# Optimization experiments

Hardware: AMD Instinct MI355X
Metric: run time of the kernel (lower is better)

## Reference

```python
import jax, jax.numpy as jnp
import numpy as np

B, N, C = 16, 2048, 128
NCLS = 40


def setup_inputs() -> dict:
    key = jax.random.key(0)
    ks = iter(jax.random.split(key, 40))

    def nrm(shape, s=0.05):
        return jax.random.normal(next(ks), shape, dtype=jnp.float32) * s

    return {
        "x": jax.random.normal(next(ks), (B, 3, N), dtype=jnp.float32),
        "conv1_w": nrm((128, 3), 0.5),
        "bn1_g": jnp.ones((128,), jnp.float32), "bn1_b": jnp.zeros((128,), jnp.float32),
        "conv2_w": nrm((128, 128)),
        "bn2_g": jnp.ones((128,), jnp.float32), "bn2_b": jnp.zeros((128,), jnp.float32),
        "sa_wqk": nrm((4, 32, 128)),
        "sa_wv": nrm((4, 128, 128)), "sa_bv": nrm((4, 128)),
        "sa_wt": nrm((4, 128, 128)), "sa_bt": nrm((4, 128)),
        "sa_g": jnp.ones((4, 128), jnp.float32), "sa_b": jnp.zeros((4, 128), jnp.float32),
        "fuse_w": nrm((1024, 512)),
        "fuse_g": jnp.ones((1024,), jnp.float32), "fuse_b": jnp.zeros((1024,), jnp.float32),
        "lin1_w": nrm((512, 1024)),
        "bn6_g": jnp.ones((512,), jnp.float32), "bn6_b": jnp.zeros((512,), jnp.float32),
        "lin2_w": nrm((256, 512)), "lin2_b": jnp.zeros((256,), jnp.float32),
        "bn7_g": jnp.ones((256,), jnp.float32), "bn7_b": jnp.zeros((256,), jnp.float32),
        "lin3_w": nrm((NCLS, 256)), "lin3_b": jnp.zeros((NCLS,), jnp.float32),
    }


def _pconv(w, x):
    # 1x1 Conv1d == channel matmul: [O,C] x [B,C,N] -> [B,O,N]
    return jnp.einsum('oc,bcn->bon', w, x)


def _fwd(x, conv1_w, bn1_g, bn1_b, conv2_w, bn2_g, bn2_b,
         sa_wqk, sa_wv, sa_bv, sa_wt, sa_bt, sa_g, sa_b,
         fuse_w, fuse_g, fuse_b, lin1_w, bn6_g, bn6_b,
         lin2_w, lin2_b, bn7_g, bn7_b, lin3_w, lin3_b):
    # conv stem (BN in eval mode: running mean=0, var=1 -> affine)
    h = jax.nn.relu(bn1_g[:, None] * _pconv(conv1_w, x) + bn1_b[:, None])
    h = jax.nn.relu(bn2_g[:, None] * _pconv(conv2_w, h) + bn2_b[:, None])

    outs = []
    for i in range(4):  # fixed number of structurally identical SA blocks
        # q_conv and k_conv share the same weight (aliased in the torch code)
        q = jnp.einsum('dc,bcn->bdn', sa_wqk[i], h)           # [B,32,N]
        energy = jnp.einsum('bdi,bdj->bij', q, q)             # [B,N,N]
        att = jax.nn.softmax(energy, axis=-1)
        att = att / (1e-9 + att.sum(axis=1, keepdims=True))   # extra L1 renorm over dim=1
        v = _pconv(sa_wv[i], h) + sa_bv[i][:, None]           # [B,C,N]
        x_r = jnp.einsum('bcn,bnm->bcm', v, att)              # [B,C,N]
        t = _pconv(sa_wt[i], h - x_r) + sa_bt[i][:, None]
        h = h + jax.nn.relu(sa_g[i][:, None] * t + sa_b[i][:, None])
        outs.append(h)

    cat = jnp.concatenate(outs, axis=1)                        # [B,512,N]
    f = fuse_g[:, None] * _pconv(fuse_w, cat) + fuse_b[:, None]
    f = jnp.where(f > 0, f, 0.2 * f)                           # LeakyReLU(0.2)
    g = f.max(axis=-1)                                         # adaptive max pool -> [B,1024]

    h1 = jax.nn.relu(bn6_g * (g @ lin1_w.T) + bn6_b)           # dropout = identity (eval)
    h2 = jax.nn.relu(bn7_g * (h1 @ lin2_w.T + lin2_b) + bn7_b)
    return h2 @ lin3_w.T + lin3_b                              # [B,40]


def reference(x, conv1_w, bn1_g, bn1_b, conv2_w, bn2_g, bn2_b,
              sa_wqk, sa_wv, sa_bv, sa_wt, sa_bt, sa_g, sa_b,
              fuse_w, fuse_g, fuse_b, lin1_w, bn6_g, bn6_b,
              lin2_w, lin2_b, bn7_g, bn7_b, lin3_w, lin3_b):
    return _fwd(x, conv1_w, bn1_g, bn1_b, conv2_w, bn2_g, bn2_b,
                sa_wqk, sa_wv, sa_bv, sa_wt, sa_bt, sa_g, sa_b,
                fuse_w, fuse_g, fuse_b, lin1_w, bn6_g, bn6_b,
                lin2_w, lin2_b, bn7_g, bn7_b, lin3_w, lin3_b)
```

## Files before the change

kernel.cpp:

```cpp
#include <hip/hip_runtime.h>

typedef __attribute__((ext_vector_type(4))) float f4;
typedef __attribute__((ext_vector_type(8))) short s16x8;
typedef __attribute__((ext_vector_type(4))) unsigned short us4;
typedef __attribute__((ext_vector_type(2))) unsigned int u32x2;
typedef unsigned short u16;
typedef unsigned int u32;

#define DEVI __device__ __forceinline__

DEVI u16 f2bf(float f){
    u32 u = __builtin_bit_cast(u32, f);
    u32 r = (u + 0x7fffu + ((u >> 16) & 1u)) >> 16;
    return (u16)r;
}
DEVI f4 mfma16(s16x8 a, s16x8 b, f4 c){
    return __builtin_amdgcn_mfma_f32_16x16x32_bf16(a, b, c, 0, 0, 0);
}
DEVI u32 cvtpk(float lo, float hi){
    u32 r;
    asm("v_cvt_pk_bf16_f32 %0, %1, %2" : "=v"(r) : "v"(lo), "v"(hi));
    return r;
}
DEVI void gload(const u16* g, u16* l){
    __builtin_amdgcn_global_load_lds((const __attribute__((address_space(1))) void*)g,
                                     (__attribute__((address_space(3))) void*)l, 16, 0, 0);
}

#define L2E 1.44269504088896340736f

__global__ __launch_bounds__(256) void k_cast(const float* w2, const float* wqk,
                                              const float* wv, const float* wt,
                                              const float* wf, u16* out){
    int i = blockIdx.x * 256 + threadIdx.x;
    if(i < 16384)       out[i] = f2bf(w2[i]);
    else if(i < 32768)  out[i] = f2bf(wqk[i - 16384]);
    else if(i < 98304)  out[i] = f2bf(wv[i - 32768]);
    else if(i < 163840) out[i] = f2bf(wt[i - 98304]);
    else if(i < 688128){
        int t = i - 163840;
        int o = t >> 9, c = t & 511;
        int jg = o >> 4, l15 = o & 15, ks = c >> 5, kr = c & 31;
        out[163840 + (size_t)(jg*16 + ks)*512 + l15*32 + kr] = f2bf(wf[t]);
    }
}

__global__ __launch_bounds__(256) void k_stem1(const float* x, const float* w1,
                                               const float* g1, const float* b1, u16* h1tb){
    int t = blockIdx.x * 256 + threadIdx.x;
    int b = t >> 11, n = t & 2047;
    const float* xb = x + (size_t)b * 3 * 2048 + n;
    float x0 = xb[0], x1 = xb[2048], x2 = xb[4096];
    u32* o = (u32*)(h1tb + (size_t)t * 128);
    #pragma unroll 8
    for(int c = 0; c < 128; c += 2){
        float a0 = fmaxf(g1[c]   * (w1[c*3+0]*x0 + w1[c*3+1]*x1 + w1[c*3+2]*x2) + b1[c],   0.f);
        float a1 = fmaxf(g1[c+1] * (w1[c*3+3]*x0 + w1[c*3+4]*x1 + w1[c*3+5]*x2) + b1[c+1], 0.f);
        o[c >> 1] = (u32)f2bf(a0) | ((u32)f2bf(a1) << 16);
    }
}

DEVI int swz512(int bid){ return ((bid & 7) << 6) | (bid >> 3); }
DEVI int swz1024(int bid){ return ((bid & 7) << 7) | (bid >> 3); }

DEVI void qv_phase(const u16* T, const u16* wqkb, const u16* wvb, const float* bv,
                   u16* qb, u16* vt, int b, int n0, int wv_, int l15, int kg){
    f4 accv[8], accq[2];
    #pragma unroll
    for(int j=0;j<8;j++) accv[j] = (f4){0.f,0.f,0.f,0.f};
    accq[0] = (f4){0.f,0.f,0.f,0.f}; accq[1] = accq[0];
    int row = wv_*16 + l15;
    #pragma unroll
    for(int ks=0; ks<4; ks++){
        s16x8 a = *(const s16x8*)&T[row*128 + ((ks*32 + kg*8) ^ ((row&7)<<3))];
        #pragma unroll
        for(int j=0;j<8;j++){
            s16x8 bb = *(const s16x8*)(wvb + (size_t)(j*16 + l15)*128 + ks*32 + kg*8);
            accv[j] = mfma16(a, bb, accv[j]);
        }
        #pragma unroll
        for(int f=0; f<2; f++){
            s16x8 wf_ = *(const s16x8*)(wqkb + (size_t)(f*16 + l15)*128 + ks*32 + kg*8);
            accq[f] = mfma16(wf_, a, accq[f]);
        }
    }
    int nb = n0 + wv_*16;
    int it = nb >> 5;
    int k0 = (nb & 31) + kg*4;
    int vbase = ((k0 >> 3)*16)*8 + (k0 & 7);
    #pragma unroll
    for(int j=0;j<8;j++){
        float bvo = bv[j*16 + l15];
        us4 pk;
        #pragma unroll
        for(int r=0;r<4;r++) pk[r] = f2bf(accv[j][r] + bvo);
        *(us4*)(vt + (size_t)((b*64 + it)*8 + j)*512 + vbase + l15*8) = pk;
    }
    int n = n0 + wv_*16 + l15;
    #pragma unroll
    for(int f=0; f<2; f++){
        us4 pk;
        #pragma unroll
        for(int r=0;r<4;r++) pk[r] = f2bf(accq[f][r]);
        *(us4*)(qb + (size_t)(b*2048 + n)*32 + f*16 + kg*4) = pk;
    }
}

__global__ __launch_bounds__(256) void k_conv2qv(const u16* h1tb, const u16* w2b,
                                                 const float* g2, const float* b2,
                                                 float* ht0,
                                                 const u16* wqkb, const u16* wvb,
                                                 const float* bv, u16* qb, u16* vt){
    __shared__ u16 T[8192];
    int bid2 = swz512(blockIdx.x);
    int b = bid2 >> 5;
    int n0 = (bid2 & 31) << 6;
    int lane = threadIdx.x & 63, wv_ = threadIdx.x >> 6;
    int l15 = lane & 15, kg = lane >> 4;
    const u16* arow = h1tb + (size_t)(b*2048 + n0 + wv_*16 + l15) * 128 + kg*8;
    f4 acc[8];
    #pragma unroll
    for(int j=0;j<8;j++) acc[j] = (f4){0.f,0.f,0.f,0.f};
    #pragma unroll
    for(int ks=0; ks<4; ks++){
        s16x8 a = *(const s16x8*)(arow + ks*32);
        #pragma unroll
        for(int j=0;j<8;j++){
            s16x8 bb = *(const s16x8*)(w2b + (size_t)(j*16 + l15)*128 + ks*32 + kg*8);
            acc[j] = mfma16(a, bb, acc[j]);
        }
    }
    int nn0 = n0 + wv_*16 + kg*4;
    #pragma unroll
    for(int j=0;j<8;j++){
        int o = j*16 + l15;
        float gg = g2[o], be = b2[o];
        #pragma unroll
        for(int r=0;r<4;r++){
            float h = fmaxf(gg * acc[j][r] + be, 0.f);
            int nl = wv_*16 + kg*4 + r;
            ht0[(size_t)(b*2048 + nn0 + r) * 128 + o] = h;
            T[nl*128 + (o ^ ((nl&7)<<3))] = f2bf(h);
        }
    }
    __syncthreads();
    qv_phase(T, wqkb, wvb, bv, qb, vt, b, n0, wv_, l15, kg);
}

__global__ __launch_bounds__(256) void k_passA(const u16* qb, float* crowp){
    int bid2 = swz1024(blockIdx.x);
    int b = bid2 >> 6;
    int rest = bid2 & 63;
    int i0 = (rest >> 1) << 6;
    int jh = rest & 1;
    int jbeg = jh << 10;
    int lane = threadIdx.x & 63, wv_ = threadIdx.x >> 6;
    int l15 = lane & 15, kg = lane >> 4;
    const u16* qbase = qb + (size_t)b * 2048 * 32;
    s16x8 af = *(const s16x8*)(qbase + (size_t)(i0 + wv_*16 + l15)*32 + kg*8);
    float m[4], s[4], mml[4];
    const f4 z = {0.f,0.f,0.f,0.f};
    {
        s16x8 b0 = *(const s16x8*)(qbase + (size_t)(jbeg + l15)*32 + kg*8);
        s16x8 b1 = *(const s16x8*)(qbase + (size_t)(jbeg + 16 + l15)*32 + kg*8);
        f4 e0 = mfma16(af, b0, z);
        f4 e1 = mfma16(af, b1, z);
        #pragma unroll
        for(int r=0;r<4;r++){
            m[r] = fmaxf(e0[r], e1[r]);
            mml[r] = -m[r]*L2E;
            s[r] = exp2f(fmaf(e0[r], L2E, mml[r])) + exp2f(fmaf(e1[r], L2E, mml[r]));
        }
    }
    for(int j0=jbeg+32; j0<jbeg+1024; j0+=32){
        s16x8 b0 = *(const s16x8*)(qbase + (size_t)(j0 + l15)*32 + kg*8);
        s16x8 b1 = *(const s16x8*)(qbase + (size_t)(j0 + 16 + l15)*32 + kg*8);
        f4 e0 = mfma16(af, b0, z);
        f4 e1 = mfma16(af, b1, z);
        #pragma unroll
        for(int r=0;r<4;r++){
            float mx = fmaxf(e0[r], e1[r]);
            if(mx > m[r] + 8.f){
                s[r] *= exp2f((m[r]-mx)*L2E);
                m[r] = mx; mml[r] = -mx*L2E;
            }
            s[r] += exp2f(fmaf(e0[r], L2E, mml[r])) + exp2f(fmaf(e1[r], L2E, mml[r]));
        }
    }
    #pragma unroll
    for(int d=1; d<16; d<<=1){
        #pragma unroll
        for(int r=0;r<4;r++){
            float mo = __shfl_xor(m[r], d);
            float so = __shfl_xor(s[r], d);
            float mn = fmaxf(m[r], mo);
            s[r] = s[r]*exp2f((m[r]-mn)*L2E) + so*exp2f((mo-mn)*L2E);
            m[r] = mn;
        }
    }
    if(l15 == 0){
        #pragma unroll
        for(int r=0;r<4;r++){
            int i = i0 + wv_*16 + kg*4 + r;
            crowp[jh*32768 + b*2048 + i] = m[r]*L2E + log2f(s[r]);
        }
    }
}

__global__ __launch_bounds__(512) void k_passB(const u16* qb, const u16* vt,
                                               const float* crowp,
                                               const float* hprev, int ldh,
                                               u16* dtb){
    __shared__ u16 V[2][8192];
    __shared__ u16 P[2][4096];
    __shared__ float CR[2048];
    __shared__ float csl[2][64];
    int bid2 = swz512(blockIdx.x);
    int b = bid2 >> 5;
    int j0 = (bid2 & 31) << 6;
    int tid = threadIdx.x;
    int lane = tid & 63, wv_ = tid >> 6;
    int jw = wv_ >> 1, ih = wv_ & 1;
    int l15 = lane & 15, kg = lane >> 4;
    int jh = jw * 16;
    const u16* qbase = qb + (size_t)b * 2048 * 32;
    const u16* vtb = vt + (size_t)b * 64*8*512;

    #pragma unroll
    for(int p=0;p<4;p++){
        int i = p*512 + tid;
        float c0 = crowp[b*2048 + i], c1 = crowp[32768 + b*2048 + i];
        float mx = fmaxf(c0, c1), mn = fminf(c0, c1);
        CR[i] = mx + log2f(1.f + exp2f(mn - mx));
    }

    s16x8 eb = *(const s16x8*)(qbase + (size_t)(j0 + jh + l15)*32 + kg*8);
    f4 acc[8];
    #pragma unroll
    for(int j=0;j<8;j++) acc[j] = (f4){0.f,0.f,0.f,0.f};
    float csp = 0.f;
    const f4 z = {0.f,0.f,0.f,0.f};

    auto stage = [&](int ic, int buf){
        const u16* src = vtb + (size_t)ic*8192 + wv_*1024 + lane*8;
        u16* dst = &V[buf][wv_*1024];
        gload(src, dst);
        gload(src + 512, dst + 512);
    };
    auto eph = [&](int ic, int buf){
        #pragma unroll
        for(int is=0; is<2; is++){
            int isub = ih*2 + is;
            s16x8 ea = *(const s16x8*)(qbase + (size_t)(ic*64 + isub*16 + l15)*32 + kg*8);
            f4 e = mfma16(ea, eb, z);
            f4 cc = *(const f4*)&CR[ic*64 + isub*16 + kg*4];
            float q0 = exp2f(fmaf(e[0], L2E, -cc[0]));
            float q1 = exp2f(fmaf(e[1], L2E, -cc[1]));
            float q2 = exp2f(fmaf(e[2], L2E, -cc[2]));
            float q3 = exp2f(fmaf(e[3], L2E, -cc[3]));
            csp += q0 + q1 + q2 + q3;
            u32x2 pk = { cvtpk(q0, q1), cvtpk(q2, q3) };
            int idx = wv_*512 + ((is*2 + (kg>>1))*16 + l15)*8 + (kg&1)*4;
            *(u32x2*)&P[buf][idx] = pk;
        }
    };

    __syncthreads();
    stage(0, 0);
    eph(0, 0);
    __syncthreads();
    for(int it=0; it<32; it++){
        int cur = it & 1;
        if(it < 31){ stage(it+1, cur^1); eph(it+1, cur^1); }
        s16x8 pa = *(const s16x8*)&P[cur][wv_*512 + lane*8];
        __builtin_amdgcn_s_setprio(1);
        #pragma unroll
        for(int jc=0;jc<8;jc++){
            s16x8 vf = *(const s16x8*)&V[cur][ih*4096 + jc*512 + lane*8];
            acc[jc] = mfma16(pa, vf, acc[jc]);
        }
        __builtin_amdgcn_s_setprio(0);
        __syncthreads();
    }
    csp += __shfl_xor(csp, 16);
    csp += __shfl_xor(csp, 32);
    if(lane < 16) csl[ih][jh + l15] = csp;
    __syncthreads();
    float* comb = (float*)V;
    if(ih == 1){
        #pragma unroll
        for(int jc=0;jc<8;jc++)
            *(f4*)&comb[jw*2048 + jc*256 + lane*4] = acc[jc];
    }
    __syncthreads();
    if(ih == 0){
        #pragma unroll
        for(int jc=0;jc<8;jc++){
            f4 o = *(const f4*)&comb[jw*2048 + jc*256 + lane*4];
            acc[jc][0] += o[0]; acc[jc][1] += o[1];
            acc[jc][2] += o[2]; acc[jc][3] += o[3];
        }
        #pragma unroll
        for(int r=0;r<4;r++){
            int jr = jh + kg*4 + r;
            float inv = 1.0f / (1e-9f + csl[0][jr] + csl[1][jr]);
            int n = j0 + jr;
            const float* hrow = hprev + (size_t)(b*2048 + n)*ldh;
            u16* drow = dtb + (size_t)(b*2048 + n)*128;
            #pragma unroll
            for(int jc=0;jc<8;jc++){
                int c = jc*16 + l15;
                drow[c] = f2bf(hrow[c] - acc[jc][r]*inv);
            }
        }
    }
}

__global__ __launch_bounds__(256) void k_tailqv(const u16* dtb, const u16* wtb, const float* bt,
                                                const float* sg, const float* sb,
                                                const float* hprev, int ldh,
                                                float* catf_o, u16* catb_o,
                                                const u16* wqkb, const u16* wvb,
                                                const float* bv, u16* qb, u16* vt, int doQV){
    __shared__ u16 T[8192];
    int bid2 = swz512(blockIdx.x);
    int b = bid2 >> 5;
    int n0 = (bid2 & 31) << 6;
    int lane = threadIdx.x & 63, wv_ = threadIdx.x >> 6;
    int l15 = lane & 15, kg = lane >> 4;
    const u16* arow = dtb + (size_t)(b*2048 + n0 + wv_*16 + l15) * 128 + kg*8;
    f4 acc[8];
    #pragma unroll
    for(int j=0;j<8;j++) acc[j] = (f4){0.f,0.f,0.f,0.f};
    #pragma unroll
    for(int ks=0; ks<4; ks++){
        s16x8 a = *(const s16x8*)(arow + ks*32);
        #pragma unroll
        for(int j=0;j<8;j++){
            s16x8 bb = *(const s16x8*)(wtb + (size_t)(j*16 + l15)*128 + ks*32 + kg*8);
            acc[j] = mfma16(a, bb, acc[j]);
        }
    }
    int nn0 = n0 + wv_*16 + kg*4;
    #pragma unroll
    for(int j=0;j<8;j++){
        int o = j*16 + l15;
        float bto = bt[o], gg = sg[o], be = sb[o];
        #pragma unroll
        for(int r=0;r<4;r++){
            int nn = nn0 + r;
            float t = acc[j][r] + bto;
            float hv = hprev[(size_t)(b*2048 + nn)*ldh + o];
            float hn = hv + fmaxf(gg*t + be, 0.f);
            size_t oi = (size_t)(b*2048 + nn)*512 + o;
            u16 hb = f2bf(hn);
            catf_o[oi] = hn;
            catb_o[oi] = hb;
            int nl = wv_*16 + kg*4 + r;
            T[nl*128 + (o ^ ((nl&7)<<3))] = hb;
        }
    }
    if(doQV){
        __syncthreads();
        qv_phase(T, wqkb, wvb, bv, qb, vt, b, n0, wv_, l15, kg);
    }
}

__global__ __launch_bounds__(512) void k_fuse(const u16* catb, const u16* wft,
                                              const float* fg, const float* fb, float* gpart){
    __shared__ u16 AB[24576];
    __shared__ float red[512];
    int bid2 = swz1024(blockIdx.x);
    int b  = bid2 >> 6;
    int rest = bid2 & 63;
    int ng = rest >> 2;
    int og = rest & 3;
    int tid = threadIdx.x;
    int lane = tid & 63, wv_ = tid >> 6;
    int wn = wv_ >> 2, wo = wv_ & 3;
    int l15 = lane & 15, kg = lane >> 4;

    f4 acc[4][4];
    #pragma unroll
    for(int mi=0;mi<4;mi++)
        #pragma unroll
        for(int j=0;j<4;j++) acc[mi][j] = (f4){0.f,0.f,0.f,0.f};

    for(int ksc=0; ksc<8; ksc++){
        if(ksc) __syncthreads();
        #pragma unroll
        for(int q=0;q<2;q++){
            int s = wv_*128 + q*64 + lane;
            int r = s >> 3;
            int c16 = (s & 7) ^ (r & 7);
            const u16* g = catb + (size_t)(b*2048 + ng*128 + r)*512 + ksc*64 + c16*8;
            gload(g, &AB[wv_*1024 + q*512]);
        }
        #pragma unroll
        for(int q=0;q<4;q++){
            int p = wv_*4 + q;
            int jgl = p >> 1, ksl = p & 1;
            const u16* g = wft + (size_t)((og*16 + jgl)*16 + ksc*2 + ksl)*512 + lane*8;
            gload(g, &AB[8192 + p*512]);
        }
        __syncthreads();
        #pragma unroll
        for(int ks=0; ks<2; ks++){
            s16x8 av[4], bw[4];
            #pragma unroll
            for(int mi=0;mi<4;mi++){
                int row = wn*64 + mi*16 + l15;
                av[mi] = *(const s16x8*)&AB[row*64 + ((ks*32 + kg*8) ^ ((row&7)<<3))];
            }
            #pragma unroll
            for(int j=0;j<4;j++){
                int p = (wo*4 + j)*2 + ks;
                bw[j] = *(const s16x8*)&AB[8192 + p*512 + l15*32 + kg*8];
            }
            #pragma unroll
            for(int j=0;j<4;j++)
                #pragma unroll
                for(int mi=0;mi<4;mi++)
                    acc[mi][j] = mfma16(av[mi], bw[j], acc[mi][j]);
        }
    }
    float vmax[4];
    #pragma unroll
    for(int j=0;j<4;j++){
        int o = og*256 + wo*64 + j*16 + l15;
        float fgv = fg[o], fbv = fb[o];
        float vm = -1e30f;
        #pragma unroll
        for(int mi=0;mi<4;mi++)
            #pragma unroll
            for(int r=0;r<4;r++){
                float f = fgv*acc[mi][j][r] + fbv;
                f = (f > 0.f) ? f : 0.2f*f;
                vm = fmaxf(vm, f);
            }
        vm = fmaxf(vm, __shfl_xor(vm, 16));
        vm = fmaxf(vm, __shfl_xor(vm, 32));
        vmax[j] = vm;
    }
    if(lane < 16){
        #pragma unroll
        for(int j=0;j<4;j++) red[(wo*2 + wn)*64 + j*16 + lane] = vmax[j];
    }
    __syncthreads();
    if(tid < 256){
        int wo2 = tid >> 6, ol = tid & 63;
        float m = fmaxf(red[(wo2*2+0)*64 + ol], red[(wo2*2+1)*64 + ol]);
        gpart[(size_t)(ng*16 + b)*1024 + og*256 + wo2*64 + ol] = m;
    }
}

__global__ __launch_bounds__(256) void k_gmax(const float* gpart, float* g){
    int i = blockIdx.x*256 + threadIdx.x;
    float m = gpart[i];
    #pragma unroll
    for(int p=1;p<16;p++) m = fmaxf(m, gpart[(size_t)p*16384 + i]);
    g[i] = m;
}

__global__ __launch_bounds__(256) void k_mlp(const float* in, const float* W, const float* bias,
                                             const float* gm, const float* bt, float* out,
                                             int IN, int OUT, int dorelu){
    int wid = blockIdx.x*4 + (threadIdx.x >> 6);
    int lane = threadIdx.x & 63;
    int b = wid / OUT, o = wid - b*OUT;
    if(b >= 16) return;
    const f4* ir = (const f4*)(in + (size_t)b*IN);
    const f4* wr = (const f4*)(W + (size_t)o*IN);
    float s = 0.f;
    for(int k=lane; k < (IN>>2); k += 64){
        f4 a = ir[k], w = wr[k];
        s += a[0]*w[0] + a[1]*w[1] + a[2]*w[2] + a[3]*w[3];
    }
    #pragma unroll
    for(int d=1; d<64; d<<=1) s += __shfl_xor(s, d);
    if(lane == 0){
        if(bias) s += bias[o];
        if(gm) s = gm[o]*s + bt[o];
        if(dorelu) s = fmaxf(s, 0.f);
        out[(size_t)b*OUT + o] = s;
    }
}

constexpr size_t OFF_WB   = 0;
constexpr size_t OFF_H1TB = 2u*1024*1024;
constexpr size_t OFF_HT0  = OFF_H1TB + 8388608;
constexpr size_t OFF_HTB0 = OFF_HT0 + 16777216;
constexpr size_t OFF_QB   = OFF_HTB0 + 8388608;
constexpr size_t OFF_VB   = OFF_QB + 2097152;
constexpr size_t OFF_CROW = OFF_VB + 8388608;
constexpr size_t OFF_GP   = OFF_CROW + 262144;
constexpr size_t OFF_DTB  = OFF_GP + 16777216 - 262144;
constexpr size_t OFF_CATF = OFF_DTB + 8388608;
constexpr size_t OFF_CATB = OFF_CATF + 67108864;
constexpr size_t OFF_G    = OFF_CATB + 33554432;
constexpr size_t OFF_H1V  = OFF_G + 65536;
constexpr size_t OFF_H2V  = OFF_H1V + 32768;

extern "C" void kernel_launch(void* const* d_in, const int* in_sizes, int n_in,
                              void* d_out, int out_size, void* d_ws, size_t ws_size,
                              hipStream_t stream){
    const float* x       = (const float*)d_in[0];
    const float* conv1_w = (const float*)d_in[1];
    const float* bn1_g   = (const float*)d_in[2];
    const float* bn1_b   = (const float*)d_in[3];
    const float* conv2_w = (const float*)d_in[4];
    const float* bn2_g   = (const float*)d_in[5];
    const float* bn2_b   = (const float*)d_in[6];
    const float* sa_wqk  = (const float*)d_in[7];
    const float* sa_wv   = (const float*)d_in[8];
    const float* sa_bv   = (const float*)d_in[9];
    const float* sa_wt   = (const float*)d_in[10];
    const float* sa_bt   = (const float*)d_in[11];
    const float* sa_g    = (const float*)d_in[12];
    const float* sa_b    = (const float*)d_in[13];
    const float* fuse_w  = (const float*)d_in[14];
    const float* fuse_g  = (const float*)d_in[15];
    const float* fuse_b  = (const float*)d_in[16];
    const float* lin1_w  = (const float*)d_in[17];
    const float* bn6_g   = (const float*)d_in[18];
    const float* bn6_b   = (const float*)d_in[19];
    const float* lin2_w  = (const float*)d_in[20];
    const float* lin2_b  = (const float*)d_in[21];
    const float* bn7_g   = (const float*)d_in[22];
    const float* bn7_b   = (const float*)d_in[23];
    const float* lin3_w  = (const float*)d_in[24];
    const float* lin3_b  = (const float*)d_in[25];

    char* ws = (char*)d_ws;
    u16*   wb    = (u16*)(ws + OFF_WB);
    u16*   h1tb  = (u16*)(ws + OFF_H1TB);
    float* ht0   = (float*)(ws + OFF_HT0);
    u16*   qbw   = (u16*)(ws + OFF_QB);
    u16*   vtw   = (u16*)(ws + OFF_VB);
    float* crowp = (float*)(ws + OFF_CROW);
    float* gpart = (float*)(ws + OFF_GP);
    u16*   dtb   = (u16*)(ws + OFF_DTB);
    float* catf  = (float*)(ws + OFF_CATF);
    u16*   catb  = (u16*)(ws + OFF_CATB);
    float* gbuf  = (float*)(ws + OFF_G);
    float* h1v   = (float*)(ws + OFF_H1V);
    float* h2v   = (float*)(ws + OFF_H2V);

    k_cast <<<2688, 256, 0, stream>>>(conv2_w, sa_wqk, sa_wv, sa_wt, fuse_w, wb);
    k_stem1<<<128,  256, 0, stream>>>(x, conv1_w, bn1_g, bn1_b, h1tb);
    k_conv2qv<<<512, 256, 0, stream>>>(h1tb, wb, bn2_g, bn2_b, ht0,
                                       wb + 16384, wb + 32768, sa_bv, qbw, vtw);

    for(int blk = 0; blk < 4; blk++){
        const float* hprev = (blk == 0) ? ht0 : (catf + (size_t)(blk-1)*128);
        int          ldh   = (blk == 0) ? 128 : 512;
        const u16* wtb  = wb + 98304 + blk*16384;
        int nb2 = (blk < 3) ? (blk + 1) : 3;
        const u16* wqkb2 = wb + 16384 + nb2*4096;
        const u16* wvb2  = wb + 32768 + nb2*16384;

        k_passA<<<1024, 256, 0, stream>>>(qbw, crowp);
        k_passB<<<512, 512, 0, stream>>>(qbw, vtw, crowp, hprev, ldh, dtb);
        k_tailqv<<<512, 256, 0, stream>>>(dtb, wtb, sa_bt + blk*128, sa_g + blk*128,
                                          sa_b + blk*128, hprev, ldh,
                                          catf + (size_t)blk*128, catb + (size_t)blk*128,
                                          wqkb2, wvb2, sa_bv + nb2*128, qbw, vtw,
                                          (blk < 3) ? 1 : 0);
    }

    k_fuse<<<1024, 512, 0, stream>>>(catb, wb + 163840, fuse_g, fuse_b, gpart);
    k_gmax<<<64,   256, 0, stream>>>(gpart, gbuf);
    k_mlp <<<2048, 256, 0, stream>>>(gbuf, lin1_w, nullptr, bn6_g, bn6_b, h1v, 1024, 512, 1);
    k_mlp <<<1024, 256, 0, stream>>>(h1v, lin2_w, lin2_b, bn7_g, bn7_b, h2v, 512, 256, 1);
    k_mlp <<<160,  256, 0, stream>>>(h2v, lin3_w, lin3_b, nullptr, nullptr,
                                     (float*)d_out, 256, 40, 0);
}
```

Before: 494.8 us.

## Double-buffer A tiles in fuse kernel and read weights directly from global

The fuse GEMM kernel now double-buffers the activation tile in LDS, prefetching the next K chunk while computing the current one, which removes one barrier per iteration. Weight fragments are loaded straight from global memory into registers instead of being staged through LDS. MFMA sections are wrapped in setprio to favour the math waves. This lowers LDS traffic and synchronization stalls, but adds global load latency on the weight path and uses more registers.

```diff
diff --git a/kernel.cpp b/kernel.cpp
--- a/kernel.cpp
+++ b/kernel.cpp
@@ -368,7 +368,7 @@
 
 __global__ __launch_bounds__(512) void k_fuse(const u16* catb, const u16* wft,
                                               const float* fg, const float* fb, float* gpart){
-    __shared__ u16 AB[24576];
+    __shared__ u16 A[2][8192];
     __shared__ float red[512];
     int bid2 = swz1024(blockIdx.x);
     int b  = bid2 >> 6;
@@ -386,43 +386,46 @@
         #pragma unroll
         for(int j=0;j<4;j++) acc[mi][j] = (f4){0.f,0.f,0.f,0.f};
 
-    for(int ksc=0; ksc<8; ksc++){
-        if(ksc) __syncthreads();
+    auto stageA = [&](int ksc, int buf){
         #pragma unroll
         for(int q=0;q<2;q++){
             int s = wv_*128 + q*64 + lane;
             int r = s >> 3;
             int c16 = (s & 7) ^ (r & 7);
             const u16* g = catb + (size_t)(b*2048 + ng*128 + r)*512 + ksc*64 + c16*8;
-            gload(g, &AB[wv_*1024 + q*512]);
-        }
-        #pragma unroll
-        for(int q=0;q<4;q++){
-            int p = wv_*4 + q;
-            int jgl = p >> 1, ksl = p & 1;
-            const u16* g = wft + (size_t)((og*16 + jgl)*16 + ksc*2 + ksl)*512 + lane*8;
-            gload(g, &AB[8192 + p*512]);
-        }
-        __syncthreads();
+            gload(g, &A[buf][wv_*1024 + q*512]);
+        }
+    };
+
+    stageA(0, 0);
+    __syncthreads();
+    for(int ksc=0; ksc<8; ksc++){
+        int cur = ksc & 1;
+        if(ksc < 7) stageA(ksc+1, cur^1);
+        s16x8 bw[2][4];
+        #pragma unroll
+        for(int ks=0; ks<2; ks++)
+            #pragma unroll
+            for(int j=0;j<4;j++)
+                bw[ks][j] = *(const s16x8*)(wft +
+                    (size_t)((og*16 + wo*4 + j)*16 + ksc*2 + ks)*512 + l15*32 + kg*8);
         #pragma unroll
         for(int ks=0; ks<2; ks++){
-            s16x8 av[4], bw[4];
+            s16x8 av[4];
             #pragma unroll
             for(int mi=0;mi<4;mi++){
                 int row = wn*64 + mi*16 + l15;
-                av[mi] = *(const s16x8*)&AB[row*64 + ((ks*32 + kg*8) ^ ((row&7)<<3))];
+                av[mi] = *(const s16x8*)&A[cur][row*64 + ((ks*32 + kg*8) ^ ((row&7)<<3))];
             }
-            #pragma unroll
-            for(int j=0;j<4;j++){
-                int p = (wo*4 + j)*2 + ks;
-                bw[j] = *(const s16x8*)&AB[8192 + p*512 + l15*32 + kg*8];
-            }
+            __builtin_amdgcn_s_setprio(1);
             #pragma unroll
             for(int j=0;j<4;j++)
                 #pragma unroll
                 for(int mi=0;mi<4;mi++)
-                    acc[mi][j] = mfma16(av[mi], bw[j], acc[mi][j]);
-        }
+                    acc[mi][j] = mfma16(av[mi], bw[ks][j], acc[mi][j]);
+            __builtin_amdgcn_s_setprio(0);
+        }
+        __syncthreads();
     }
     float vmax[4];
     #pragma unroll
```

Result: no change. 503.9 us (+1.8%).

## Fuse SA tail and next-block QV projection into attention passB kernel

Applied to the files above, without the earlier changes.

Merges the passB attention-value kernel with the trans-conv/residual tail and the next block's Q/V projection. The bf16 difference tile now stays in shared memory instead of making a global round trip through dtb, and one launch per SA block is removed. Q/V buffers are double-buffered so passB can write the next block's Q/V while still reading the current ones. The fuse-weight layout is also permuted so the B-fragment is read contiguously per lane. In exchange, the fused kernel carries more work per block and only 4 MFMA columns per wave in the tail.

```diff
diff --git a/kernel.cpp b/kernel.cpp
--- a/kernel.cpp
+++ b/kernel.cpp
@@ -41,7 +41,7 @@
         int t = i - 163840;
         int o = t >> 9, c = t & 511;
         int jg = o >> 4, l15 = o & 15, ks = c >> 5, kr = c & 31;
-        out[163840 + (size_t)(jg*16 + ks)*512 + l15*32 + kr] = f2bf(wf[t]);
+        out[163840 + (size_t)(jg*16 + ks)*512 + ((kr>>3)*16 + l15)*8 + (kr&7)] = f2bf(wf[t]);
     }
 }
 
@@ -207,10 +207,15 @@
     }
 }
 
-__global__ __launch_bounds__(512) void k_passB(const u16* qb, const u16* vt,
-                                               const float* crowp,
-                                               const float* hprev, int ldh,
-                                               u16* dtb){
+__global__ __launch_bounds__(512) void k_passBT(const u16* qb, const u16* vt,
+                                                const float* crowp,
+                                                const float* hprev, int ldh,
+                                                const u16* wtb, const float* bt,
+                                                const float* sg, const float* sb,
+                                                float* catf_o, u16* catb_o,
+                                                const u16* wqkb2, const u16* wvb2,
+                                                const float* bv2,
+                                                u16* qb2, u16* vt2, int doQV){
     __shared__ u16 V[2][8192];
     __shared__ u16 P[2][4096];
     __shared__ float CR[2048];
@@ -293,6 +298,7 @@
             *(f4*)&comb[jw*2048 + jc*256 + lane*4] = acc[jc];
     }
     __syncthreads();
+    u16* Td = (u16*)P;
     if(ih == 0){
         #pragma unroll
         for(int jc=0;jc<8;jc++){
@@ -306,63 +312,85 @@
             float inv = 1.0f / (1e-9f + csl[0][jr] + csl[1][jr]);
             int n = j0 + jr;
             const float* hrow = hprev + (size_t)(b*2048 + n)*ldh;
-            u16* drow = dtb + (size_t)(b*2048 + n)*128;
             #pragma unroll
             for(int jc=0;jc<8;jc++){
                 int c = jc*16 + l15;
-                drow[c] = f2bf(hrow[c] - acc[jc][r]*inv);
+                Td[jr*128 + (c ^ ((jr&7)<<3))] = f2bf(hrow[c] - acc[jc][r]*inv);
             }
         }
     }
-}
-
-__global__ __launch_bounds__(256) void k_tailqv(const u16* dtb, const u16* wtb, const float* bt,
-                                                const float* sg, const float* sb,
-                                                const float* hprev, int ldh,
-                                                float* catf_o, u16* catb_o,
-                                                const u16* wqkb, const u16* wvb,
-                                                const float* bv, u16* qb, u16* vt, int doQV){
-    __shared__ u16 T[8192];
-    int bid2 = swz512(blockIdx.x);
-    int b = bid2 >> 5;
-    int n0 = (bid2 & 31) << 6;
-    int lane = threadIdx.x & 63, wv_ = threadIdx.x >> 6;
-    int l15 = lane & 15, kg = lane >> 4;
-    const u16* arow = dtb + (size_t)(b*2048 + n0 + wv_*16 + l15) * 128 + kg*8;
-    f4 acc[8];
-    #pragma unroll
-    for(int j=0;j<8;j++) acc[j] = (f4){0.f,0.f,0.f,0.f};
-    #pragma unroll
-    for(int ks=0; ks<4; ks++){
-        s16x8 a = *(const s16x8*)(arow + ks*32);
-        #pragma unroll
-        for(int j=0;j<8;j++){
-            s16x8 bb = *(const s16x8*)(wtb + (size_t)(j*16 + l15)*128 + ks*32 + kg*8);
-            acc[j] = mfma16(a, bb, acc[j]);
-        }
-    }
-    int nn0 = n0 + wv_*16 + kg*4;
-    #pragma unroll
-    for(int j=0;j<8;j++){
-        int o = j*16 + l15;
+    __syncthreads();
+    f4 accT[4];
+    #pragma unroll
+    for(int j2=0;j2<4;j2++) accT[j2] = (f4){0.f,0.f,0.f,0.f};
+    {
+        int arow_l = jh + l15;
+        #pragma unroll
+        for(int ks=0; ks<4; ks++){
+            s16x8 a = *(const s16x8*)&Td[arow_l*128 + ((ks*32 + kg*8) ^ ((arow_l&7)<<3))];
+            #pragma unroll
+            for(int j2=0;j2<4;j2++){
+                int o = ih*64 + j2*16 + l15;
+                s16x8 bb = *(const s16x8*)(wtb + (size_t)o*128 + ks*32 + kg*8);
+                accT[j2] = mfma16(a, bb, accT[j2]);
+            }
+        }
+    }
+    u16* T2 = (u16*)V;
+    #pragma unroll
+    for(int j2=0;j2<4;j2++){
+        int o = ih*64 + j2*16 + l15;
         float bto = bt[o], gg = sg[o], be = sb[o];
         #pragma unroll
         for(int r=0;r<4;r++){
-            int nn = nn0 + r;
-            float t = acc[j][r] + bto;
-            float hv = hprev[(size_t)(b*2048 + nn)*ldh + o];
+            int jr = jh + kg*4 + r;
+            int n = j0 + jr;
+            float t = accT[j2][r] + bto;
+            float hv = hprev[(size_t)(b*2048 + n)*ldh + o];
             float hn = hv + fmaxf(gg*t + be, 0.f);
-            size_t oi = (size_t)(b*2048 + nn)*512 + o;
+            size_t oi = (size_t)(b*2048 + n)*512 + o;
             u16 hb = f2bf(hn);
             catf_o[oi] = hn;
             catb_o[oi] = hb;
-            int nl = wv_*16 + kg*4 + r;
-            T[nl*128 + (o ^ ((nl&7)<<3))] = hb;
-        }
-    }
+            T2[jr*128 + (o ^ ((jr&7)<<3))] = hb;
+        }
+    }
+    __syncthreads();
     if(doQV){
-        __syncthreads();
-        qv_phase(T, wqkb, wvb, bv, qb, vt, b, n0, wv_, l15, kg);
+        f4 accv[4], accq;
+        #pragma unroll
+        for(int jj=0;jj<4;jj++) accv[jj] = (f4){0.f,0.f,0.f,0.f};
+        accq = (f4){0.f,0.f,0.f,0.f};
+        int row = jh + l15;
+        #pragma unroll
+        for(int ks=0; ks<4; ks++){
+            s16x8 a = *(const s16x8*)&T2[row*128 + ((ks*32 + kg*8) ^ ((row&7)<<3))];
+            #pragma unroll
+            for(int jj=0;jj<4;jj++){
+                s16x8 bb = *(const s16x8*)(wvb2 + (size_t)((ih*4+jj)*16 + l15)*128 + ks*32 + kg*8);
+                accv[jj] = mfma16(a, bb, accv[jj]);
+            }
+            s16x8 wf_ = *(const s16x8*)(wqkb2 + (size_t)(ih*16 + l15)*128 + ks*32 + kg*8);
+            accq = mfma16(wf_, a, accq);
+        }
+        int nb = j0 + jh;
+        int it2 = nb >> 5;
+        int k0 = (nb & 31) + kg*4;
+        int vbase = ((k0 >> 3)*16)*8 + (k0 & 7);
+        #pragma unroll
+        for(int jj=0;jj<4;jj++){
+            int jc4 = ih*4 + jj;
+            float bvo = bv2[jc4*16 + l15];
+            us4 pk;
+            #pragma unroll
+            for(int r=0;r<4;r++) pk[r] = f2bf(accv[jj][r] + bvo);
+            *(us4*)(vt2 + (size_t)((b*64 + it2)*8 + jc4)*512 + vbase + l15*8) = pk;
+        }
+        int n = j0 + jh + l15;
+        us4 pk;
+        #pragma unroll
+        for(int r=0;r<4;r++) pk[r] = f2bf(accq[r]);
+        *(us4*)(qb2 + (size_t)(b*2048 + n)*32 + ih*16 + kg*4) = pk;
     }
 }
 
@@ -415,7 +443,7 @@
             #pragma unroll
             for(int j=0;j<4;j++){
                 int p = (wo*4 + j)*2 + ks;
-                bw[j] = *(const s16x8*)&AB[8192 + p*512 + l15*32 + kg*8];
+                bw[j] = *(const s16x8*)&AB[8192 + p*512 + lane*8];
             }
             #pragma unroll
             for(int j=0;j<4;j++)
@@ -486,18 +514,19 @@
     }
 }
 
+constexpr size_t MB = 1048576;
 constexpr size_t OFF_WB   = 0;
-constexpr size_t OFF_H1TB = 2u*1024*1024;
-constexpr size_t OFF_HT0  = OFF_H1TB + 8388608;
-constexpr size_t OFF_HTB0 = OFF_HT0 + 16777216;
-constexpr size_t OFF_QB   = OFF_HTB0 + 8388608;
-constexpr size_t OFF_VB   = OFF_QB + 2097152;
-constexpr size_t OFF_CROW = OFF_VB + 8388608;
-constexpr size_t OFF_GP   = OFF_CROW + 262144;
-constexpr size_t OFF_DTB  = OFF_GP + 16777216 - 262144;
-constexpr size_t OFF_CATF = OFF_DTB + 8388608;
-constexpr size_t OFF_CATB = OFF_CATF + 67108864;
-constexpr size_t OFF_G    = OFF_CATB + 33554432;
+constexpr size_t OFF_H1TB = 2*MB;
+constexpr size_t OFF_HT0  = 10*MB;
+constexpr size_t OFF_QB0  = 26*MB;
+constexpr size_t OFF_QB1  = 28*MB;
+constexpr size_t OFF_VB0  = 30*MB;
+constexpr size_t OFF_VB1  = 38*MB;
+constexpr size_t OFF_CROW = 46*MB;
+constexpr size_t OFF_GP   = 46*MB + 262144;
+constexpr size_t OFF_CATF = 48*MB;
+constexpr size_t OFF_CATB = 112*MB;
+constexpr size_t OFF_G    = 144*MB;
 constexpr size_t OFF_H1V  = OFF_G + 65536;
 constexpr size_t OFF_H2V  = OFF_H1V + 32768;
 
@@ -535,11 +564,10 @@
     u16*   wb    = (u16*)(ws + OFF_WB);
     u16*   h1tb  = (u16*)(ws + OFF_H1TB);
     float* ht0   = (float*)(ws + OFF_HT0);
-    u16*   qbw   = (u16*)(ws + OFF_QB);
-    u16*   vtw   = (u16*)(ws + OFF_VB);
+    u16*   qbb[2] = { (u16*)(ws + OFF_QB0), (u16*)(ws + OFF_QB1) };
+    u16*   vtb[2] = { (u16*)(ws + OFF_VB0), (u16*)(ws + OFF_VB1) };
     float* crowp = (float*)(ws + OFF_CROW);
     float* gpart = (float*)(ws + OFF_GP);
-    u16*   dtb   = (u16*)(ws + OFF_DTB);
     float* catf  = (float*)(ws + OFF_CATF);
     u16*   catb  = (u16*)(ws + OFF_CATB);
     float* gbuf  = (float*)(ws + OFF_G);
@@ -549,9 +577,10 @@
     k_cast <<<2688, 256, 0, stream>>>(conv2_w, sa_wqk, sa_wv, sa_wt, fuse_w, wb);
     k_stem1<<<128,  256, 0, stream>>>(x, conv1_w, bn1_g, bn1_b, h1tb);
     k_conv2qv<<<512, 256, 0, stream>>>(h1tb, wb, bn2_g, bn2_b, ht0,
-                                       wb + 16384, wb + 32768, sa_bv, qbw, vtw);
+                                       wb + 16384, wb + 32768, sa_bv, qbb[0], vtb[0]);
 
     for(int blk = 0; blk < 4; blk++){
+        int cur = blk & 1, nxt = cur ^ 1;
         const float* hprev = (blk == 0) ? ht0 : (catf + (size_t)(blk-1)*128);
         int          ldh   = (blk == 0) ? 128 : 512;
         const u16* wtb  = wb + 98304 + blk*16384;
@@ -559,13 +588,12 @@
         const u16* wqkb2 = wb + 16384 + nb2*4096;
         const u16* wvb2  = wb + 32768 + nb2*16384;
 
-        k_passA<<<1024, 256, 0, stream>>>(qbw, crowp);
-        k_passB<<<512, 512, 0, stream>>>(qbw, vtw, crowp, hprev, ldh, dtb);
-        k_tailqv<<<512, 256, 0, stream>>>(dtb, wtb, sa_bt + blk*128, sa_g + blk*128,
-                                          sa_b + blk*128, hprev, ldh,
+        k_passA<<<1024, 256, 0, stream>>>(qbb[cur], crowp);
+        k_passBT<<<512, 512, 0, stream>>>(qbb[cur], vtb[cur], crowp, hprev, ldh,
+                                          wtb, sa_bt + blk*128, sa_g + blk*128, sa_b + blk*128,
                                           catf + (size_t)blk*128, catb + (size_t)blk*128,
-                                          wqkb2, wvb2, sa_bv + nb2*128, qbw, vtw,
-                                          (blk < 3) ? 1 : 0);
+                                          wqkb2, wvb2, sa_bv + nb2*128,
+                                          qbb[nxt], vtb[nxt], (blk < 3) ? 1 : 0);
     }
 
     k_fuse<<<1024, 512, 0, stream>>>(catb, wb + 163840, fuse_g, fuse_b, gpart);
```

Result: faster. 459.4 us (-7.2%).
